# Optimization experiments

Hardware: AMD Instinct MI355X
Metric: run time of the kernel (lower is better)

The kernel has to match this reference:

```python
import jax, jax.numpy as jnp
import numpy as np

B, H, W, C = 2, 128, 128, 256
WS = 8            # current_window (query window)
KW = 16           # halo_window = 2*current_window
HEADS = 8
HD = C // HEADS
PRETRAIN = 8
CPB_HIDDEN = 512


def _rel_bias_consts():
    halo = (KW - WS) // 2
    coords = np.arange(1 - WS - halo, WS + halo, dtype=np.float32)  # length WS+KW-1 = 23
    tab = np.stack(np.meshgrid(coords, coords, indexing='ij'), axis=-1)  # [23,23,2]
    tab = tab * (8.0 / (PRETRAIN - 1.0))
    tab = np.sign(tab) * np.log1p(np.abs(tab)) / np.log(8.0)
    tab = tab.reshape(-1, 2).astype(np.float32)                      # [529,2]
    qi = np.arange(WS)
    qg = np.stack(np.meshgrid(qi, qi, indexing='ij')).reshape(2, -1)  # [2,64]
    ki = np.arange(KW)
    kg = np.stack(np.meshgrid(ki, ki, indexing='ij')).reshape(2, -1)  # [2,256]
    rel = qg[:, :, None] - kg[:, None] + (KW - 1)
    idx = (rel[0] * (WS + KW - 1) + rel[1]).reshape(-1).astype(np.int32)  # [64*256]
    return tab, idx

_REL_TAB, _REL_IDX = _rel_bias_consts()


def setup_inputs() -> dict:
    key = jax.random.key(0)
    ks = jax.random.split(key, 12)
    s = 0.02
    return {
        'x': jax.random.normal(ks[0], (B, H, W, C), jnp.float32),
        'w_qkv': jax.random.normal(ks[1], (C, 3 * C), jnp.float32) * s,
        'w_dw': jax.random.normal(ks[2], (3, 3, 1, 3 * C), jnp.float32) * s,  # depthwise HWIO
        'ln_g': jnp.ones((3 * C,), jnp.float32),
        'ln_b': jnp.zeros((3 * C,), jnp.float32),
        'q_bias': jnp.zeros((C,), jnp.float32),
        'v_bias': jnp.zeros((C,), jnp.float32),
        'logit_scale': jnp.full((HEADS, 1, 1), np.log(10.0), jnp.float32),
        'cpb_w1': jax.random.normal(ks[3], (2, CPB_HIDDEN), jnp.float32) * s,
        'cpb_b1': jnp.zeros((CPB_HIDDEN,), jnp.float32),
        'cpb_w2': jax.random.normal(ks[4], (CPB_HIDDEN, HEADS), jnp.float32) * s,
        'w_proj': jax.random.normal(ks[5], (C, C), jnp.float32) * s,
    }


def _l2n(t):
    # tf.math.l2_normalize with epsilon=1.55e-5
    return t * jax.lax.rsqrt(jnp.maximum(jnp.sum(t * t, -1, keepdims=True), 1.55e-5))


def reference(x, w_qkv, w_dw, ln_g, ln_b, q_bias, v_bias, logit_scale,
              cpb_w1, cpb_b1, cpb_w2, w_proj):
    nWh, nWw = H // WS, W // WS
    nW = nWh * nWw
    # qkv 1x1 conv + depthwise 3x3 + layernorm + (q,0,v) bias
    qkv = jnp.einsum('bhwc,cd->bhwd', x, w_qkv)
    qkv = jax.lax.conv_general_dilated(
        qkv, w_dw, (1, 1), 'SAME',
        dimension_numbers=('NHWC', 'HWIO', 'NHWC'), feature_group_count=3 * C)
    mu = jnp.mean(qkv, -1, keepdims=True)
    var = jnp.var(qkv, -1, keepdims=True)
    qkv = (qkv - mu) * jax.lax.rsqrt(var + 1e-5) * ln_g + ln_b
    qkv = qkv + jnp.concatenate([q_bias, jnp.zeros_like(q_bias), v_bias])
    q, kv = qkv[..., :C], qkv[..., C:]
    # window partition of q: [B*nW, heads, WS*WS, HD]
    qp = q.reshape(B, nWh, WS, nWw, WS, HEADS, HD)
    qp = qp.transpose(0, 1, 3, 5, 2, 4, 6).reshape(B * nW, HEADS, WS * WS, HD)
    # halo partition of kv: overlapping KWxKW patches, stride WS
    halo = (KW - WS) // 2
    kvp = jnp.pad(kv, ((0, 0), (halo, halo), (halo, halo), (0, 0)))
    ridx = (np.arange(nWh) * WS)[:, None] + np.arange(KW)[None]  # [nWh,KW]
    cidx = (np.arange(nWw) * WS)[:, None] + np.arange(KW)[None]  # [nWw,KW]
    kvp = kvp[:, ridx][:, :, :, cidx]               # [B,nWh,KW,nWw,KW,2C]
    kvp = kvp.transpose(0, 1, 3, 2, 4, 5).reshape(B * nW, KW * KW, 2, HEADS, HD)
    k = kvp[:, :, 0].transpose(0, 2, 1, 3)          # [B*nW, heads, KW*KW, HD]
    v = kvp[:, :, 1].transpose(0, 2, 1, 3)
    # cosine attention with clamped learned log-scale
    scale = jnp.exp(jnp.minimum(logit_scale, np.float32(np.log(100.0))))
    attn = jnp.einsum('whqd,whkd->whqk', _l2n(qp) * scale, _l2n(k))
    # continuous relative position bias (CPB MLP + gather)
    hidden = jax.nn.relu(jnp.asarray(_REL_TAB) @ cpb_w1 + cpb_b1)
    bias_tab = jax.nn.sigmoid(hidden @ cpb_w2) * 16.0        # [529, heads]
    rb = bias_tab[_REL_IDX].reshape(WS * WS, KW * KW, HEADS).transpose(2, 0, 1)
    attn = jax.nn.softmax(attn + rb[None], axis=-1)
    out = jnp.einsum('whqk,whkd->whqd', attn, v)             # [B*nW, heads, 64, HD]
    # reverse window partition
    out = out.reshape(B, nWh, nWw, HEADS, WS, WS, HD)
    out = out.transpose(0, 1, 4, 2, 5, 3, 6).reshape(B, H, W, C)
    return jnp.einsum('bhwc,cd->bhwd', out, w_proj)
```

## Files before the change

### kernel.cpp

```cpp
#include <hip/hip_runtime.h>
#include <hip/hip_bf16.h>
#include <hip/hip_fp16.h>
#include <cstddef>
#include <cstdint>

#define BB 2
#define HH 128
#define WW 128
#define CC 256
#define WSZ 8
#define KWIN 16
#define NHEADS 8
#define HD 32
#define C3 768
#define NPIX 32768
#define NWIN 512

typedef short    bf16x8 __attribute__((ext_vector_type(8)));
typedef _Float16 half8  __attribute__((ext_vector_type(8)));
typedef float    f32x4  __attribute__((ext_vector_type(4)));

__device__ inline short f2bf(float f) {
    union { float f; unsigned u; } v; v.f = f;
    unsigned r = (v.u + 0x7fffu + ((v.u >> 16) & 1u)) >> 16;
    return (short)r;
}

__device__ inline void gload_lds16(const _Float16* g, _Float16* l) {
    __builtin_amdgcn_global_load_lds(
        (const __attribute__((address_space(1))) unsigned int*)g,
        (__attribute__((address_space(3))) unsigned int*)l, 16, 0, 0);
}

__global__ __launch_bounds__(64) void cpb_kernel(const float* __restrict__ w1,
                                                 const float* __restrict__ b1,
                                                 const float* __restrict__ w2,
                                                 float* __restrict__ btab) {
    const int e = blockIdx.x;
    const int i = e / 23, j = e % 23;
    const float inv_log8 = 1.0f / logf(8.0f);
    float c0 = (float)(i - 11) * (8.0f / 7.0f);
    float c1 = (float)(j - 11) * (8.0f / 7.0f);
    float f0 = copysignf(log1pf(fabsf(c0)) * inv_log8, c0);
    float f1 = copysignf(log1pf(fabsf(c1)) * inv_log8, c1);

    const int t = threadIdx.x;
    float acc[8] = {0.f,0.f,0.f,0.f,0.f,0.f,0.f,0.f};
    for (int kk = 0; kk < 8; kk++) {
        int k = kk * 64 + t;
        float hid = f0 * w1[k] + f1 * w1[512 + k] + b1[k];
        hid = fmaxf(hid, 0.f);
        #pragma unroll
        for (int h = 0; h < 8; h++) acc[h] += hid * w2[k * 8 + h];
    }
    #pragma unroll
    for (int h = 0; h < 8; h++) {
        #pragma unroll
        for (int off = 32; off >= 1; off >>= 1) acc[h] += __shfl_xor(acc[h], off);
    }
    if (t < 8) {
        float v = acc[t];
        btab[e * 8 + t] = 16.0f / (1.0f + expf(-v));
    }
}

__global__ __launch_bounds__(256) void cvt_wdw(const float* __restrict__ src,
                                               _Float16* __restrict__ dst) {
    int i = blockIdx.x * 256 + threadIdx.x;
    if (i < 9 * C3) dst[i] = (_Float16)src[i];
}

__global__ __launch_bounds__(256) void transpose_cvt(const float* __restrict__ src,
                                                     _Float16* __restrict__ dst,
                                                     int R, int Cn) {
    __shared__ float t[32][33];
    const int bx = blockIdx.x, by = blockIdx.y;
    const int tx = threadIdx.x & 31, ty = threadIdx.x >> 5;
    #pragma unroll
    for (int i = 0; i < 4; i++) {
        int r = by * 32 + ty + i * 8;
        t[ty + i * 8][tx] = src[(size_t)r * Cn + bx * 32 + tx];
    }
    __syncthreads();
    #pragma unroll
    for (int i = 0; i < 4; i++) {
        int dr = bx * 32 + ty + i * 8;
        dst[(size_t)dr * R + by * 32 + tx] = (_Float16)t[tx][ty + i * 8];
    }
}

template <typename OT>
__global__ __launch_bounds__(256) void gemm_f16(const _Float16* __restrict__ A,
                                                const _Float16* __restrict__ Bt,
                                                OT* __restrict__ C,
                                                int M, int N, int K) {
    __shared__ _Float16 Ash[128][64];
    __shared__ _Float16 Bsh[128][64];
    const int tid = threadIdx.x;
    const int wv = tid >> 6, ln = tid & 63;
    const int quad = ln >> 4, l15 = ln & 15;
    const int rowb = blockIdx.y * 128;
    const int colb = blockIdx.x * 128;
    const int wm = (wv >> 1) * 64, wn = (wv & 1) * 64;

    const int r8 = ln >> 3, g = ln & 7;
    const int kg = g ^ r8;

    f32x4 acc[4][4] = {};
    for (int k0 = 0; k0 < K; k0 += 64) {
        #pragma unroll
        for (int i = 0; i < 4; i++) {
            const int m = wv * 32 + i * 8 + r8;
            gload_lds16(A + (size_t)(rowb + m) * K + k0 + kg * 8,
                        &Ash[wv * 32 + i * 8][0]);
            gload_lds16(Bt + (size_t)(colb + m) * K + k0 + kg * 8,
                        &Bsh[wv * 32 + i * 8][0]);
        }
        __syncthreads();
        #pragma unroll
        for (int kk = 0; kk < 2; kk++) {
            const int phys = ((kk * 4 + quad) ^ (l15 & 7)) * 8;
            half8 a[4], b[4];
            #pragma unroll
            for (int i = 0; i < 4; i++)
                a[i] = *(const half8*)&Ash[wm + i * 16 + l15][phys];
            #pragma unroll
            for (int j = 0; j < 4; j++)
                b[j] = *(const half8*)&Bsh[wn + j * 16 + l15][phys];
            #pragma unroll
            for (int i = 0; i < 4; i++)
                #pragma unroll
                for (int j = 0; j < 4; j++)
                    acc[i][j] = __builtin_amdgcn_mfma_f32_16x16x32_f16(
                        a[i], b[j], acc[i][j], 0, 0, 0);
        }
        __syncthreads();
    }
    #pragma unroll
    for (int i = 0; i < 4; i++) {
        #pragma unroll
        for (int reg = 0; reg < 4; reg++) {
            const size_t row = rowb + wm + i * 16 + quad * 4 + reg;
            #pragma unroll
            for (int j = 0; j < 4; j++) {
                C[row * N + colb + wn + j * 16 + l15] = (OT)acc[i][j][reg];
            }
        }
    }
}

__global__ __launch_bounds__(256) void gemm_qkv(const float* __restrict__ A,
                                                const _Float16* __restrict__ Bt,
                                                _Float16* __restrict__ C,
                                                int M, int N, int K) {
    __shared__ _Float16 Ash[128][64];
    __shared__ _Float16 Bsh[128][64];
    const int tid = threadIdx.x;
    const int wv = tid >> 6, ln = tid & 63;
    const int quad = ln >> 4, l15 = ln & 15;
    const int rowb = blockIdx.y * 128;
    const int colb = blockIdx.x * 128;
    const int wm = (wv >> 1) * 64, wn = (wv & 1) * 64;
    const int r8 = ln >> 3, g = ln & 7;
    const int kg = g ^ r8;

    f32x4 acc[4][4] = {};
    for (int k0 = 0; k0 < K; k0 += 64) {
        #pragma unroll
        for (int i = 0; i < 4; i++) {
            const int m = wv * 32 + i * 8 + r8;
            const float* ap = A + (size_t)(rowb + m) * K + k0 + g * 8;
            const float4 a0 = *(const float4*)ap;
            const float4 a1 = *(const float4*)(ap + 4);
            half8 hv;
            hv[0] = (_Float16)a0.x; hv[1] = (_Float16)a0.y;
            hv[2] = (_Float16)a0.z; hv[3] = (_Float16)a0.w;
            hv[4] = (_Float16)a1.x; hv[5] = (_Float16)a1.y;
            hv[6] = (_Float16)a1.z; hv[7] = (_Float16)a1.w;
            *(half8*)&Ash[wv * 32 + i * 8 + r8][kg * 8] = hv;
            gload_lds16(Bt + (size_t)(colb + m) * K + k0 + kg * 8,
                        &Bsh[wv * 32 + i * 8][0]);
        }
        __syncthreads();
        #pragma unroll
        for (int kk = 0; kk < 2; kk++) {
            const int phys = ((kk * 4 + quad) ^ (l15 & 7)) * 8;
            half8 a[4], b[4];
            #pragma unroll
            for (int i = 0; i < 4; i++)
                a[i] = *(const half8*)&Ash[wm + i * 16 + l15][phys];
            #pragma unroll
            for (int j = 0; j < 4; j++)
                b[j] = *(const half8*)&Bsh[wn + j * 16 + l15][phys];
            #pragma unroll
            for (int i = 0; i < 4; i++)
                #pragma unroll
                for (int j = 0; j < 4; j++)
                    acc[i][j] = __builtin_amdgcn_mfma_f32_16x16x32_f16(
                        a[i], b[j], acc[i][j], 0, 0, 0);
        }
        __syncthreads();
    }
    #pragma unroll
    for (int i = 0; i < 4; i++) {
        #pragma unroll
        for (int reg = 0; reg < 4; reg++) {
            const size_t row = rowb + wm + i * 16 + quad * 4 + reg;
            #pragma unroll
            for (int j = 0; j < 4; j++) {
                C[row * N + colb + wn + j * 16 + l15] = (_Float16)acc[i][j][reg];
            }
        }
    }
}

__global__ __launch_bounds__(256) void dwconv_ln(const _Float16* __restrict__ in,
                                                 const _Float16* __restrict__ wdwh,
                                                 const float* __restrict__ g,
                                                 const float* __restrict__ bt,
                                                 const float* __restrict__ qb,
                                                 const float* __restrict__ vb,
                                                 _Float16* __restrict__ out) {
    __shared__ _Float16 S[2880 * 8];
    __shared__ float sred[4][8][2];

    const int t = threadIdx.x;
    const int pix0 = blockIdx.x * 8;
    const int b = pix0 >> 14, y = (pix0 >> 7) & 127, x0 = pix0 & 127;

    for (int u = t; u < 2880; u += 256) {
        const int r = u / 960, rem = u - r * 960;
        const int c = rem / 96, grp = rem - c * 96;
        const int yy = y + r - 1, xx = x0 + c - 1;
        half8 v = (half8)(_Float16)0;
        if ((unsigned)yy < 128u && (unsigned)xx < 128u)
            v = *(const half8*)(in + (((size_t)(b * 128 + yy) * 128 + xx) * C3)
                                + grp * 8);
        const int phys = (u & ~7) | ((u ^ c) & 7);
        *(half8*)&S[phys * 8] = v;
    }
    __syncthreads();

    const int p = t & 7, gidx = t >> 3;
    float acc[3][8] = {};
    #pragma unroll
    for (int s = 0; s < 3; s++) {
        const int grp = gidx + s * 32;
        half8 w[9];
        #pragma unroll
        for (int tap = 0; tap < 9; tap++)
            w[tap] = *(const half8*)(wdwh + (tap * 96 + grp) * 8);
        #pragma unroll
        for (int r = 0; r < 3; r++) {
            #pragma unroll
            for (int dx = 0; dx < 3; dx++) {
                const int c = p + dx;
                const int u = (r * 10 + c) * 96 + grp;
                const int phys = (u & ~7) | ((u ^ c) & 7);
                const half8 v = *(const half8*)&S[phys * 8];
                const half8 wt = w[r * 3 + dx];
                #pragma unroll
                for (int i = 0; i < 8; i++)
                    acc[s][i] += (float)v[i] * (float)wt[i];
            }
        }
    }

    float ls = 0.f, lss = 0.f;
    #pragma unroll
    for (int s = 0; s < 3; s++)
        #pragma unroll
        for (int i = 0; i < 8; i++) { ls += acc[s][i]; lss += acc[s][i] * acc[s][i]; }
    ls  += __shfl_xor(ls, 8);  lss += __shfl_xor(lss, 8);
    ls  += __shfl_xor(ls, 16); lss += __shfl_xor(lss, 16);
    ls  += __shfl_xor(ls, 32); lss += __shfl_xor(lss, 32);
    const int wv = t >> 6, lnid = t & 63;
    if (lnid < 8) { sred[wv][lnid][0] = ls; sred[wv][lnid][1] = lss; }
    __syncthreads();
    const float Ssum  = sred[0][p][0] + sred[1][p][0] + sred[2][p][0] + sred[3][p][0];
    const float SSsum = sred[0][p][1] + sred[1][p][1] + sred[2][p][1] + sred[3][p][1];
    const float mu  = Ssum * (1.0f / 768.0f);
    const float var = SSsum * (1.0f / 768.0f) - mu * mu;
    const float rs  = rsqrtf(var + 1e-5f);

    const size_t obase = (size_t)(pix0 + p) * C3;
    #pragma unroll
    for (int s = 0; s < 3; s++) {
        const int ch = gidx * 8 + s * 256;
        const float4 g0 = *(const float4*)(g + ch);
        const float4 g1 = *(const float4*)(g + ch + 4);
        const float4 b0 = *(const float4*)(bt + ch);
        const float4 b1 = *(const float4*)(bt + ch + 4);
        float gg[8] = {g0.x, g0.y, g0.z, g0.w, g1.x, g1.y, g1.z, g1.w};
        float bb[8] = {b0.x, b0.y, b0.z, b0.w, b1.x, b1.y, b1.z, b1.w};
        if (s == 0) {
            const float4 e0 = *(const float4*)(qb + ch);
            const float4 e1 = *(const float4*)(qb + ch + 4);
            bb[0] += e0.x; bb[1] += e0.y; bb[2] += e0.z; bb[3] += e0.w;
            bb[4] += e1.x; bb[5] += e1.y; bb[6] += e1.z; bb[7] += e1.w;
        } else if (s == 2) {
            const float4 e0 = *(const float4*)(vb + ch - 512);
            const float4 e1 = *(const float4*)(vb + ch - 512 + 4);
            bb[0] += e0.x; bb[1] += e0.y; bb[2] += e0.z; bb[3] += e0.w;
            bb[4] += e1.x; bb[5] += e1.y; bb[6] += e1.z; bb[7] += e1.w;
        }
        if (s == 2) {
            bf16x8 o;
            #pragma unroll
            for (int i = 0; i < 8; i++)
                o[i] = f2bf((acc[s][i] - mu) * rs * gg[i] + bb[i]);
            *(bf16x8*)((short*)(out + obase + ch)) = o;
        } else {
            half8 o;
            #pragma unroll
            for (int i = 0; i < 8; i++)
                o[i] = (_Float16)((acc[s][i] - mu) * rs * gg[i] + bb[i]);
            *(half8*)(out + obase + ch) = o;
        }
    }
}

__global__ __launch_bounds__(256) void attn_mfma(const _Float16* __restrict__ qkv,
                                                 const float* __restrict__ bias_tab,
                                                 const float* __restrict__ logit_scale,
                                                 _Float16* __restrict__ out) {
    const int blk = blockIdx.x;
    const int h = blk & 7;
    const int wid = blk >> 3;
    const int b = wid >> 8;
    const int wy = (wid >> 4) & 15;
    const int wx = wid & 15;
    const int tid = threadIdx.x;
    const int wave = tid >> 6, lane = tid & 63;
    const int quad = lane >> 4, l15 = lane & 15;

    __shared__ _Float16 Bf[16 * 64 * 8];
    __shared__ short Vt[32][264];
    __shared__ short Pl[4][16][128];
    __shared__ float btab[529];

    const float lscale = __expf(fminf(logit_scale[h], 4.60517019f));
    const float Mshift = lscale + 16.0f;
    for (int e = tid; e < 529; e += 256) btab[e] = bias_tab[e * 8 + h] - Mshift;

    {
        const int j = tid;
        const int kr = j >> 4, kcc = j & 15;
        const int gy = wy * 8 - 4 + kr, gx = wx * 8 - 4 + kcc;
        const bool inb = ((unsigned)gy < 128u) && ((unsigned)gx < 128u);
        const _Float16* p = qkv +
            (((size_t)(b * 128 + (inb ? gy : 0)) * 128 + (inb ? gx : 0)) * C3) +
            256 + h * HD;
        const short* vp = (const short*)(p + 256);
        float kreg[32];
        float s2 = 0.f;
        #pragma unroll
        for (int d8 = 0; d8 < 4; d8++) {
            half8 kk;
            bf16x8 vv;
            if (inb) { kk = *(const half8*)(p + d8 * 8); vv = *(const bf16x8*)(vp + d8 * 8); }
            else     { kk = (half8)(_Float16)0;          vv = (bf16x8)(short)0; }
            #pragma unroll
            for (int u = 0; u < 8; u++) {
                const float kf = (float)kk[u];
                kreg[d8 * 8 + u] = kf;
                s2 += kf * kf;
                Vt[d8 * 8 + u][j] = vv[u];
            }
        }
        const float r = rsqrtf(fmaxf(s2, 1.55e-5f));
        #pragma unroll
        for (int d8 = 0; d8 < 4; d8++) {
            half8 hv;
            #pragma unroll
            for (int u = 0; u < 8; u++)
                hv[u] = (_Float16)(kreg[d8 * 8 + u] * r);
            *(half8*)&Bf[(((j >> 4) * 64) + d8 * 16 + (j & 15)) * 8] = hv;
        }
    }
    __syncthreads();

    const int qrow = wave * 16 + l15;
    const int qr = qrow >> 3, qc = qrow & 7;
    const int qy = wy * 8 + qr, qx = wx * 8 + qc;
    half8 afrag;
    {
        const _Float16* qp = qkv + (((size_t)(b * 128 + qy) * 128 + qx) * C3) + h * HD + quad * 8;
        half8 q8 = *(const half8*)qp;
        float qf[8];
        float s2 = 0.f;
        #pragma unroll
        for (int u = 0; u < 8; u++) { qf[u] = (float)q8[u]; s2 += qf[u] * qf[u]; }
        s2 += __shfl_xor(s2, 16);
        s2 += __shfl_xor(s2, 32);
        const float rq = rsqrtf(fmaxf(s2, 1.55e-5f)) * lscale;
        #pragma unroll
        for (int u = 0; u < 8; u++) afrag[u] = (_Float16)(qf[u] * rq);
    }

    float lsum[4] = {0.f, 0.f, 0.f, 0.f};
    f32x4 d0 = {0.f, 0.f, 0.f, 0.f};
    f32x4 d1 = {0.f, 0.f, 0.f, 0.f};
    #pragma unroll
    for (int hf = 0; hf < 2; hf++) {
        #pragma unroll
        for (int ntl = 0; ntl < 8; ntl++) {
            const int nt = hf * 8 + ntl;
            half8 bfrag = *(const half8*)&Bf[(nt * 64 + lane) * 8];
            f32x4 s = {0.f, 0.f, 0.f, 0.f};
            s = __builtin_amdgcn_mfma_f32_16x16x32_f16(afrag, bfrag, s, 0, 0, 0);
            #pragma unroll
            for (int reg = 0; reg < 4; reg++) {
                const int q  = quad * 4 + reg;
                const int gq = wave * 16 + q;
                const int rqr = gq >> 3, rqc = gq & 7;
                const float rb = btab[(rqr - nt + 15) * 23 + (rqc - l15 + 15)];
                const float pv = __expf(s[reg] + rb);
                lsum[reg] += pv;
                Pl[wave][q][(ntl * 16 + l15) ^ ((q & 12) << 2)] = f2bf(pv);
            }
        }
        #pragma unroll
        for (int ch = 0; ch < 4; ch++) {
            const int kb = hf * 128 + ch * 32;
            bf16x8 pa = *(const bf16x8*)&Pl[wave][l15][(ch * 32 + quad * 8) ^ ((l15 & 12) << 2)];
            bf16x8 b0 = *(const bf16x8*)&Vt[l15][kb + quad * 8];
            bf16x8 b1 = *(const bf16x8*)&Vt[l15 + 16][kb + quad * 8];
            d0 = __builtin_amdgcn_mfma_f32_16x16x32_bf16(pa, b0, d0, 0, 0, 0);
            d1 = __builtin_amdgcn_mfma_f32_16x16x32_bf16(pa, b1, d1, 0, 0, 0);
        }
    }
    #pragma unroll
    for (int reg = 0; reg < 4; reg++) {
        float v = lsum[reg];
        v += __shfl_xor(v, 1); v += __shfl_xor(v, 2);
        v += __shfl_xor(v, 4); v += __shfl_xor(v, 8);
        lsum[reg] = 1.0f / v;
    }

    #pragma unroll
    for (int reg = 0; reg < 4; reg++) {
        const int gq = wave * 16 + quad * 4 + reg;
        const int oqr = gq >> 3, oqc = gq & 7;
        const int oy = wy * 8 + oqr, ox = wx * 8 + oqc;
        _Float16* op = out + (((size_t)(b * 128 + oy) * 128 + ox) * CC) + h * HD;
        op[l15]      = (_Float16)(d0[reg] * lsum[reg]);
        op[16 + l15] = (_Float16)(d1[reg] * lsum[reg]);
    }
}

extern "C" void kernel_launch(void* const* d_in, const int* in_sizes, int n_in,
                              void* d_out, int out_size, void* d_ws, size_t ws_size,
                              hipStream_t stream) {
    const float* x           = (const float*)d_in[0];
    const float* w_qkv       = (const float*)d_in[1];
    const float* w_dw        = (const float*)d_in[2];
    const float* ln_g        = (const float*)d_in[3];
    const float* ln_b        = (const float*)d_in[4];
    const float* q_bias      = (const float*)d_in[5];
    const float* v_bias      = (const float*)d_in[6];
    const float* logit_scale = (const float*)d_in[7];
    const float* cpb_w1      = (const float*)d_in[8];
    const float* cpb_b1      = (const float*)d_in[9];
    const float* cpb_w2      = (const float*)d_in[10];
    const float* w_proj      = (const float*)d_in[11];
    float* out = (float*)d_out;

    char* ws = (char*)d_ws;
    _Float16* qkv0h  = (_Float16*)(ws);
    _Float16* qkvh   = (_Float16*)(ws + 50331648);
    _Float16* attnh  = (_Float16*)(ws + 100663296);
    _Float16* wqkvT  = (_Float16*)(ws + 117440512);
    _Float16* wprojT = (_Float16*)(ws + 117833728);
    _Float16* wdwh   = (_Float16*)(ws + 117964800);
    float*    btab   = (float*)   (ws + 117981184);

    cpb_kernel<<<529, 64, 0, stream>>>(cpb_w1, cpb_b1, cpb_w2, btab);
    cvt_wdw<<<27, 256, 0, stream>>>(w_dw, wdwh);
    transpose_cvt<<<dim3(C3 / 32, CC / 32), 256, 0, stream>>>(w_qkv, wqkvT, CC, C3);
    transpose_cvt<<<dim3(CC / 32, CC / 32), 256, 0, stream>>>(w_proj, wprojT, CC, CC);

    gemm_qkv<<<dim3(C3 / 128, NPIX / 128), 256, 0, stream>>>(
        x, wqkvT, qkv0h, NPIX, C3, CC);
    dwconv_ln<<<NPIX / 8, 256, 0, stream>>>(qkv0h, wdwh, ln_g, ln_b, q_bias,
                                            v_bias, qkvh);
    attn_mfma<<<NWIN * NHEADS, 256, 0, stream>>>(qkvh, btab, logit_scale, attnh);
    gemm_f16<float><<<dim3(CC / 128, NPIX / 128), 256, 0, stream>>>(
        attnh, wprojT, out, NPIX, CC, CC);
}
```

Baseline: 251.1 us.

## Keep attention probabilities in registers via transposed QK MFMA and exp2 softmax

The QK^T MFMA now takes K as the A operand and Q as the B operand, with K stored in LDS in a permuted layout. The resulting score fragment then matches the A-operand layout of the PV MFMA, so the per-wave LDS staging buffer for P and its write/read round trip are removed. Softmax switches to exp2 with log2e folded into the Q scale and bias table, plus a constant shift so fp16 probabilities keep precision. V is now stored as fp16 instead of bf16 so the PV MFMA is f16, and the row-sum reduction needs fewer shuffles. The risks are fp16 overflow or underflow of unnormalised probabilities and reduced accuracy for V.

```diff
diff --git a/kernel.cpp b/kernel.cpp
--- a/kernel.cpp
+++ b/kernel.cpp
@@ -20,11 +20,13 @@
 typedef _Float16 half8  __attribute__((ext_vector_type(8)));
 typedef float    f32x4  __attribute__((ext_vector_type(4)));
 
-__device__ inline short f2bf(float f) {
-    union { float f; unsigned u; } v; v.f = f;
-    unsigned r = (v.u + 0x7fffu + ((v.u >> 16) & 1u)) >> 16;
-    return (short)r;
-}
+#define LOG2E 1.4426950408889634f
+
+#if __has_builtin(__builtin_amdgcn_exp2f)
+#define EXP2(x) __builtin_amdgcn_exp2f(x)
+#else
+#define EXP2(x) __expf((x) * 0.6931471805599453f)
+#endif
 
 __device__ inline void gload_lds16(const _Float16* g, _Float16* l) {
     __builtin_amdgcn_global_load_lds(
@@ -304,21 +306,15 @@
             bb[0] += e0.x; bb[1] += e0.y; bb[2] += e0.z; bb[3] += e0.w;
             bb[4] += e1.x; bb[5] += e1.y; bb[6] += e1.z; bb[7] += e1.w;
         }
-        if (s == 2) {
-            bf16x8 o;
-            #pragma unroll
-            for (int i = 0; i < 8; i++)
-                o[i] = f2bf((acc[s][i] - mu) * rs * gg[i] + bb[i]);
-            *(bf16x8*)((short*)(out + obase + ch)) = o;
-        } else {
-            half8 o;
-            #pragma unroll
-            for (int i = 0; i < 8; i++)
-                o[i] = (_Float16)((acc[s][i] - mu) * rs * gg[i] + bb[i]);
-            *(half8*)(out + obase + ch) = o;
-        }
-    }
-}
+        half8 o;
+        #pragma unroll
+        for (int i = 0; i < 8; i++)
+            o[i] = (_Float16)((acc[s][i] - mu) * rs * gg[i] + bb[i]);
+        *(half8*)(out + obase + ch) = o;
+    }
+}
+
+#define P2SHIFT 14.0f
 
 __global__ __launch_bounds__(256) void attn_mfma(const _Float16* __restrict__ qkv,
                                                  const float* __restrict__ bias_tab,
@@ -334,14 +330,14 @@
     const int wave = tid >> 6, lane = tid & 63;
     const int quad = lane >> 4, l15 = lane & 15;
 
-    __shared__ _Float16 Bf[16 * 64 * 8];
-    __shared__ short Vt[32][264];
-    __shared__ short Pl[4][16][128];
+    __shared__ __align__(16) _Float16 Bf[16 * 64 * 8];
+    __shared__ __align__(16) _Float16 Vt[32][264];
     __shared__ float btab[529];
 
     const float lscale = __expf(fminf(logit_scale[h], 4.60517019f));
-    const float Mshift = lscale + 16.0f;
-    for (int e = tid; e < 529; e += 256) btab[e] = bias_tab[e * 8 + h] - Mshift;
+    const float MshiftL2 = (lscale + 16.0f) * LOG2E - P2SHIFT;
+    for (int e = tid; e < 529; e += 256)
+        btab[e] = bias_tab[e * 8 + h] * LOG2E - MshiftL2;
 
     {
         const int j = tid;
@@ -351,15 +347,13 @@
         const _Float16* p = qkv +
             (((size_t)(b * 128 + (inb ? gy : 0)) * 128 + (inb ? gx : 0)) * C3) +
             256 + h * HD;
-        const short* vp = (const short*)(p + 256);
         float kreg[32];
         float s2 = 0.f;
         #pragma unroll
         for (int d8 = 0; d8 < 4; d8++) {
-            half8 kk;
-            bf16x8 vv;
-            if (inb) { kk = *(const half8*)(p + d8 * 8); vv = *(const bf16x8*)(vp + d8 * 8); }
-            else     { kk = (half8)(_Float16)0;          vv = (bf16x8)(short)0; }
+            half8 kk, vv;
+            if (inb) { kk = *(const half8*)(p + d8 * 8); vv = *(const half8*)(p + 256 + d8 * 8); }
+            else     { kk = (half8)(_Float16)0;          vv = (half8)(_Float16)0; }
             #pragma unroll
             for (int u = 0; u < 8; u++) {
                 const float kf = (float)kk[u];
@@ -369,21 +363,22 @@
             }
         }
         const float r = rsqrtf(fmaxf(s2, 1.55e-5f));
+        const int nt  = ((j >> 5) << 1) | ((j >> 2) & 1);
+        const int pos = (((j >> 3) & 3) << 2) | (j & 3);
         #pragma unroll
         for (int d8 = 0; d8 < 4; d8++) {
             half8 hv;
             #pragma unroll
             for (int u = 0; u < 8; u++)
                 hv[u] = (_Float16)(kreg[d8 * 8 + u] * r);
-            *(half8*)&Bf[(((j >> 4) * 64) + d8 * 16 + (j & 15)) * 8] = hv;
-        }
-    }
-    __syncthreads();
+            *(half8*)&Bf[((nt * 64) + d8 * 16 + pos) * 8] = hv;
+        }
+    }
 
     const int qrow = wave * 16 + l15;
     const int qr = qrow >> 3, qc = qrow & 7;
     const int qy = wy * 8 + qr, qx = wx * 8 + qc;
-    half8 afrag;
+    half8 qfrag;
     {
         const _Float16* qp = qkv + (((size_t)(b * 128 + qy) * 128 + qx) * C3) + h * HD + quad * 8;
         half8 q8 = *(const half8*)qp;
@@ -393,59 +388,55 @@
         for (int u = 0; u < 8; u++) { qf[u] = (float)q8[u]; s2 += qf[u] * qf[u]; }
         s2 += __shfl_xor(s2, 16);
         s2 += __shfl_xor(s2, 32);
-        const float rq = rsqrtf(fmaxf(s2, 1.55e-5f)) * lscale;
-        #pragma unroll
-        for (int u = 0; u < 8; u++) afrag[u] = (_Float16)(qf[u] * rq);
-    }
-
-    float lsum[4] = {0.f, 0.f, 0.f, 0.f};
+        const float rq = rsqrtf(fmaxf(s2, 1.55e-5f)) * lscale * LOG2E;
+        #pragma unroll
+        for (int u = 0; u < 8; u++) qfrag[u] = (_Float16)(qf[u] * rq);
+    }
+    __syncthreads();
+
+    const int colbase = qc + 15 - ((quad & 1) << 3);
+    const int rowq    = qr + 15 - (quad >> 1);
+    float lsum = 0.f;
     f32x4 d0 = {0.f, 0.f, 0.f, 0.f};
     f32x4 d1 = {0.f, 0.f, 0.f, 0.f};
     #pragma unroll
-    for (int hf = 0; hf < 2; hf++) {
-        #pragma unroll
-        for (int ntl = 0; ntl < 8; ntl++) {
-            const int nt = hf * 8 + ntl;
-            half8 bfrag = *(const half8*)&Bf[(nt * 64 + lane) * 8];
-            f32x4 s = {0.f, 0.f, 0.f, 0.f};
-            s = __builtin_amdgcn_mfma_f32_16x16x32_f16(afrag, bfrag, s, 0, 0, 0);
-            #pragma unroll
-            for (int reg = 0; reg < 4; reg++) {
-                const int q  = quad * 4 + reg;
-                const int gq = wave * 16 + q;
-                const int rqr = gq >> 3, rqc = gq & 7;
-                const float rb = btab[(rqr - nt + 15) * 23 + (rqc - l15 + 15)];
-                const float pv = __expf(s[reg] + rb);
-                lsum[reg] += pv;
-                Pl[wave][q][(ntl * 16 + l15) ^ ((q & 12) << 2)] = f2bf(pv);
-            }
-        }
-        #pragma unroll
-        for (int ch = 0; ch < 4; ch++) {
-            const int kb = hf * 128 + ch * 32;
-            bf16x8 pa = *(const bf16x8*)&Pl[wave][l15][(ch * 32 + quad * 8) ^ ((l15 & 12) << 2)];
-            bf16x8 b0 = *(const bf16x8*)&Vt[l15][kb + quad * 8];
-            bf16x8 b1 = *(const bf16x8*)&Vt[l15 + 16][kb + quad * 8];
-            d0 = __builtin_amdgcn_mfma_f32_16x16x32_bf16(pa, b0, d0, 0, 0, 0);
-            d1 = __builtin_amdgcn_mfma_f32_16x16x32_bf16(pa, b1, d1, 0, 0, 0);
-        }
-    }
+    for (int ch = 0; ch < 8; ch++) {
+        const half8 ka0 = *(const half8*)&Bf[((2 * ch)     * 64 + lane) * 8];
+        const half8 ka1 = *(const half8*)&Bf[((2 * ch + 1) * 64 + lane) * 8];
+        f32x4 s0 = {0.f, 0.f, 0.f, 0.f};
+        f32x4 s1 = {0.f, 0.f, 0.f, 0.f};
+        s0 = __builtin_amdgcn_mfma_f32_16x16x32_f16(ka0, qfrag, s0, 0, 0, 0);
+        s1 = __builtin_amdgcn_mfma_f32_16x16x32_f16(ka1, qfrag, s1, 0, 0, 0);
+        const float* bt = &btab[(rowq - 2 * ch) * 23 + colbase];
+        half8 pa;
+        #pragma unroll
+        for (int r = 0; r < 4; r++) {
+            const float p0 = EXP2(s0[r] + bt[-r]);
+            const float p1 = EXP2(s1[r] + bt[-4 - r]);
+            lsum += p0 + p1;
+            pa[r]     = (_Float16)p0;
+            pa[4 + r] = (_Float16)p1;
+        }
+        const half8 v0 = *(const half8*)&Vt[l15][ch * 32 + quad * 8];
+        const half8 v1 = *(const half8*)&Vt[l15 + 16][ch * 32 + quad * 8];
+        d0 = __builtin_amdgcn_mfma_f32_16x16x32_f16(pa, v0, d0, 0, 0, 0);
+        d1 = __builtin_amdgcn_mfma_f32_16x16x32_f16(pa, v1, d1, 0, 0, 0);
+    }
+
+    lsum += __shfl_xor(lsum, 16);
+    lsum += __shfl_xor(lsum, 32);
+    const float inv = 1.0f / lsum;
+
     #pragma unroll
     for (int reg = 0; reg < 4; reg++) {
-        float v = lsum[reg];
-        v += __shfl_xor(v, 1); v += __shfl_xor(v, 2);
-        v += __shfl_xor(v, 4); v += __shfl_xor(v, 8);
-        lsum[reg] = 1.0f / v;
-    }
-
-    #pragma unroll
-    for (int reg = 0; reg < 4; reg++) {
-        const int gq = wave * 16 + quad * 4 + reg;
+        const int q = quad * 4 + reg;
+        const float invq = __shfl(inv, q);
+        const int gq = wave * 16 + q;
         const int oqr = gq >> 3, oqc = gq & 7;
         const int oy = wy * 8 + oqr, ox = wx * 8 + oqc;
         _Float16* op = out + (((size_t)(b * 128 + oy) * 128 + ox) * CC) + h * HD;
-        op[l15]      = (_Float16)(d0[reg] * lsum[reg]);
-        op[16 + l15] = (_Float16)(d1[reg] * lsum[reg]);
+        op[l15]      = (_Float16)(d0[reg] * invq);
+        op[16 + l15] = (_Float16)(d1[reg] * invq);
     }
 }
 
```

Result: faster. 245.5 us (-2.2%).
